# Kernel optimization log

Measured on AMD Instinct MI355X. Metric: run time of the kernel, lower is better.

Reference implementation:

```python
import jax, jax.numpy as jnp
import numpy as np

# dims: T time steps, B batch, F clinical features, H GRU hidden, NH heads, DFF ffn dim, AH single-attn hidden
T, B, F, H, NH, DFF, AH = 128, 256, 76, 64, 4, 256, 8


def setup_inputs() -> dict:
    key = jax.random.key(0)
    ks = jax.random.split(key, 32)
    s = 0.1
    def u(k, shape):
        return jax.random.uniform(k, shape, jnp.float32, -s, s)
    return {
        "x": jax.random.normal(ks[0], (T, B, F), jnp.float32),
        # per-feature GRU(1, H) weight stacks (torch gate order: r, z, n)
        "gru_w_ih": u(ks[1], (F, 3 * H)),          # input dim is 1 -> squeezed
        "gru_w_hh": u(ks[2], (F, 3 * H, H)),
        "gru_b_ih": jnp.zeros((F, 3 * H), jnp.float32),
        "gru_b_hh": jnp.zeros((F, 3 * H), jnp.float32),
        # per-feature SingleAttention('new', time_aware) params
        "att_Wt": u(ks[3], (F, H, AH)),
        "att_Wx": u(ks[4], (F, H, AH)),
        "att_rate": jnp.full((F,), 0.8, jnp.float32),
        # multi-head self-attention over the feature axis
        "mha_wq": u(ks[5], (H, H)), "mha_bq": jnp.zeros((H,), jnp.float32),
        "mha_wk": u(ks[6], (H, H)), "mha_bk": jnp.zeros((H,), jnp.float32),
        "mha_wv": u(ks[7], (H, H)), "mha_bv": jnp.zeros((H,), jnp.float32),
        "mha_wo": u(ks[8], (H, H)), "mha_bo": jnp.zeros((H,), jnp.float32),
        # position-wise feed forward
        "ffn_w1": u(ks[9], (H, DFF)), "ffn_b1": jnp.zeros((DFF,), jnp.float32),
        "ffn_w2": u(ks[10], (DFF, H)), "ffn_b2": jnp.zeros((H,), jnp.float32),
        # FinalAttentionQKV ('mul')
        "fa_wq": u(ks[11], (H, H)), "fa_bq": jnp.zeros((H,), jnp.float32),
        "fa_wk": u(ks[12], (H, H)), "fa_bk": jnp.zeros((H,), jnp.float32),
        "fa_wv": u(ks[13], (H, H)), "fa_bv": jnp.zeros((H,), jnp.float32),
        # output head
        "out0_w": u(ks[14], (H, H)), "out0_b": jnp.zeros((H,), jnp.float32),
        "out1_w": u(ks[15], (H, 1)), "out1_b": jnp.zeros((1,), jnp.float32),
    }


def reference(x, gru_w_ih, gru_w_hh, gru_b_ih, gru_b_hh,
              att_Wt, att_Wx, att_rate,
              mha_wq, mha_bq, mha_wk, mha_bk, mha_wv, mha_bv, mha_wo, mha_bo,
              ffn_w1, ffn_b1, ffn_w2, ffn_b2,
              fa_wq, fa_bq, fa_wk, fa_bk, fa_wv, fa_bv,
              out0_w, out0_b, out1_w, out1_b):
    # x: (T, B, F); torch permutes to (B, T, F)
    Ts, Bsz, Fd = x.shape
    Hd = gru_w_hh.shape[-1]
    dk = Hd // NH

    # ---- all F GRU(1,H) channels fused into one scan (vectorized over F) ----
    xs = jnp.transpose(x, (0, 2, 1))  # (T, F, B)

    def step(h, x_t):  # h: (F,B,H), x_t: (F,B)
        gx = x_t[:, :, None] * gru_w_ih[:, None, :] + gru_b_ih[:, None, :]      # (F,B,3H)
        gh = jnp.einsum('fbh,fgh->fbg', h, gru_w_hh) + gru_b_hh[:, None, :]     # (F,B,3H)
        rx, zx, nx = jnp.split(gx, 3, axis=-1)
        rh, zh, nh = jnp.split(gh, 3, axis=-1)
        r = jax.nn.sigmoid(rx + rh)
        z = jax.nn.sigmoid(zx + zh)
        n = jnp.tanh(nx + r * nh)
        h_new = (1.0 - z) * n + z * h
        return h_new, h_new

    h0 = jnp.zeros((Fd, Bsz, Hd), x.dtype)
    _, hs = jax.lax.scan(step, h0, xs)        # (T, F, B, H)
    hs = jnp.transpose(hs, (1, 2, 0, 3))       # (F, B, T, H)

    # ---- per-feature SingleAttention, type='new', time-aware ----
    q = jnp.einsum('fbh,fha->fba', hs[:, :, -1, :], att_Wt)   # (F,B,AH)
    k = jnp.einsum('fbth,fha->fbta', hs, att_Wx)              # (F,B,T,AH)
    dp = jnp.einsum('fba,fbta->fbt', q, k)                    # (F,B,T)
    sig = jax.nn.sigmoid(dp)
    decay = jnp.arange(Ts, 0, -1, dtype=x.dtype)              # T..1 (time_decays + 1)
    denom = jax.nn.sigmoid(att_rate)[:, None, None] * (jnp.log(2.72 + (1.0 - sig)) * decay)
    e = jax.nn.relu(sig / denom)
    a = jax.nn.softmax(e, axis=-1)
    emb = jnp.einsum('fbt,fbth->bfh', a, hs)                  # (B, F, H)

    def lin(t, w, b):
        return t @ w + b

    # ---- multi-head self-attention over the F axis + residual ----
    # NOTE: original lambda ignores its (layernormed) argument, so LN is dead code.
    def heads(t):
        return t.reshape(Bsz, Fd, NH, dk).transpose(0, 2, 1, 3)
    qh = heads(lin(emb, mha_wq, mha_bq))
    kh = heads(lin(emb, mha_wk, mha_bk))
    vh = heads(lin(emb, mha_wv, mha_bv))
    scores = jnp.einsum('bhqd,bhkd->bhqk', qh, kh) / jnp.sqrt(jnp.asarray(dk, x.dtype))
    attn = jax.nn.softmax(scores, axis=-1)
    ctx = jnp.einsum('bhqk,bhkd->bhqd', attn, vh).transpose(0, 2, 1, 3).reshape(Bsz, Fd, Hd)
    ctx = emb + lin(ctx, mha_wo, mha_bo)

    # ---- position-wise feed-forward + residual ----
    ctx = ctx + lin(jax.nn.relu(lin(ctx, ffn_w1, ffn_b1)), ffn_w2, ffn_b2)

    # ---- FinalAttentionQKV, type='mul' ----
    fq = lin(ctx[:, -1, :], fa_wq, fa_bq)      # (B,H)
    fk = lin(ctx, fa_wk, fa_bk)                # (B,F,H)
    fv = lin(ctx, fa_wv, fa_bv)                # (B,F,H)
    fe = jnp.einsum('bfh,bh->bf', fk, fq)
    fa_w = jax.nn.softmax(fe, axis=1)
    v = jnp.einsum('bf,bfh->bh', fa_w, fv)     # (B,H)

    # ---- output head ----
    out = jax.nn.sigmoid(lin(jax.nn.relu(lin(v, out0_w, out0_b)), out1_w, out1_b))
    return out  # (B, 1)
```

## Files before the change

kernel.cpp:

```cpp
#include <hip/hip_runtime.h>
#include <hip/hip_bf16.h>
#include <cstdint>
#include <cstddef>

#define TT 128
#define BBATCH 256
#define FFEAT 76
#define HDIM 64
#define NHEAD 4
#define DKH 16
#define DFF1 256
#define AH1 8
#define NROWS (BBATCH * FFEAT)
#define FCP 38

#define LOG2E 1.4426950408889634f

typedef __attribute__((ext_vector_type(8))) short bf16x8;
typedef __attribute__((ext_vector_type(4))) float f32x4;

__device__ __forceinline__ float fast_sigmoid(float v) {
    float p = __builtin_amdgcn_exp2f(-v * LOG2E);
    return __builtin_amdgcn_rcpf(1.0f + p);
}
__device__ __forceinline__ float fast_tanh(float v) {
    float p = __builtin_amdgcn_exp2f(v * (2.0f * LOG2E));
    return 1.0f - 2.0f * __builtin_amdgcn_rcpf(1.0f + p);
}
__device__ __forceinline__ short f2bf(float x) {
    __hip_bfloat16 h = __float2bfloat16(x);
    return *reinterpret_cast<short*>(&h);
}
__device__ __forceinline__ float bf2f(unsigned short s) {
    return __uint_as_float(((unsigned)s) << 16);
}
__device__ __forceinline__ unsigned pack_bf16(float a, float b) {
    unsigned ua = (unsigned)(unsigned short)f2bf(a);
    unsigned ub = (unsigned)(unsigned short)f2bf(b);
    return ua | (ub << 16);
}

__device__ __forceinline__ void attn_wave(
    __hip_bfloat16* hs_chunk, const float* Wt, const float* Wx,
    const float* rate, int f, int f_loc, int b, int lane)
{
    const int g = lane >> 3;
    const int i = lane & 7;
    short* rowbase = (short*)hs_chunk + ((size_t)f_loc * BBATCH + b) * TT * HDIM;
    const uint4* basev = (const uint4*)rowbase;

    uint4 U[16];
    #pragma unroll
    for (int it = 0; it < 16; ++it)
        U[it] = basev[(it * 8 + g) * 8 + i];

    float qv[8];
    {
        uint4 Uv = U[15];
        float h15[8];
        h15[0]=__uint_as_float(Uv.x<<16); h15[1]=__uint_as_float(Uv.x&0xffff0000u);
        h15[2]=__uint_as_float(Uv.y<<16); h15[3]=__uint_as_float(Uv.y&0xffff0000u);
        h15[4]=__uint_as_float(Uv.z<<16); h15[5]=__uint_as_float(Uv.z&0xffff0000u);
        h15[6]=__uint_as_float(Uv.w<<16); h15[7]=__uint_as_float(Uv.w&0xffff0000u);
        const float* wtp = Wt + (size_t)f * 512 + (size_t)(8 * i) * 8;
        #pragma unroll
        for (int a = 0; a < 8; ++a) qv[a] = 0.f;
        #pragma unroll
        for (int j = 0; j < 8; ++j)
            #pragma unroll
            for (int a = 0; a < 8; ++a)
                qv[a] = fmaf(h15[j], wtp[j * 8 + a], qv[a]);
        #pragma unroll
        for (int a = 0; a < 8; ++a) {
            qv[a] += __shfl_xor(qv[a], 1, 64);
            qv[a] += __shfl_xor(qv[a], 2, 64);
            qv[a] += __shfl_xor(qv[a], 4, 64);
            qv[a]  = __shfl(qv[a], 63, 64);
        }
    }
    float wv[8];
    {
        const float* wxp = Wx + (size_t)f * 512 + (size_t)(8 * i) * 8;
        #pragma unroll
        for (int j = 0; j < 8; ++j) {
            float s2 = 0.f;
            #pragma unroll
            for (int a = 0; a < 8; ++a) s2 = fmaf(wxp[j * 8 + a], qv[a], s2);
            wv[j] = s2;
        }
    }
    const float rs = fast_sigmoid(rate[f]);

    float m = -1.0e30f, s = 0.f;
    float o[8];
    #pragma unroll
    for (int j = 0; j < 8; ++j) o[j] = 0.f;

    #pragma unroll
    for (int it = 0; it < 16; ++it) {
        const int t = it * 8 + g;
        uint4 Uv = U[it];
        float h[8];
        h[0] = __uint_as_float(Uv.x << 16); h[1] = __uint_as_float(Uv.x & 0xffff0000u);
        h[2] = __uint_as_float(Uv.y << 16); h[3] = __uint_as_float(Uv.y & 0xffff0000u);
        h[4] = __uint_as_float(Uv.z << 16); h[5] = __uint_as_float(Uv.z & 0xffff0000u);
        h[6] = __uint_as_float(Uv.w << 16); h[7] = __uint_as_float(Uv.w & 0xffff0000u);
        float dp = 0.f;
        #pragma unroll
        for (int j = 0; j < 8; ++j) dp = fmaf(h[j], wv[j], dp);
        dp += __shfl_xor(dp, 1, 64);
        dp += __shfl_xor(dp, 2, 64);
        dp += __shfl_xor(dp, 4, 64);
        float sig = fast_sigmoid(dp);
        float den = rs * (__logf(2.72f + (1.0f - sig)) * (float)(TT - t));
        float e = fmaxf(sig / den, 0.0f);
        float nm = fmaxf(m, e);
        float sc = __builtin_amdgcn_exp2f((m - nm) * LOG2E);
        float p  = __builtin_amdgcn_exp2f((e - nm) * LOG2E);
        s = fmaf(s, sc, p);
        #pragma unroll
        for (int j = 0; j < 8; ++j) o[j] = fmaf(o[j], sc, p * h[j]);
        m = nm;
    }
    #pragma unroll
    for (int k = 8; k <= 32; k <<= 1) {
        float om = __shfl_xor(m, k, 64);
        float os = __shfl_xor(s, k, 64);
        float nm = fmaxf(m, om);
        float sa = __builtin_amdgcn_exp2f((m - nm) * LOG2E);
        float sb = __builtin_amdgcn_exp2f((om - nm) * LOG2E);
        s = s * sa + os * sb;
        #pragma unroll
        for (int j = 0; j < 8; ++j) {
            float oo = __shfl_xor(o[j], k, 64);
            o[j] = o[j] * sa + oo * sb;
        }
        m = nm;
    }
    if (g == 0) {
        float inv = __builtin_amdgcn_rcpf(s);
        float4 v0, v1;
        v0.x = o[0]*inv; v0.y = o[1]*inv; v0.z = o[2]*inv; v0.w = o[3]*inv;
        v1.x = o[4]*inv; v1.y = o[5]*inv; v1.z = o[6]*inv; v1.w = o[7]*inv;
        float* edst = (float*)rowbase;
        *(float4*)&edst[8 * i]     = v0;
        *(float4*)&edst[8 * i + 4] = v1;
    }
}

__global__ __launch_bounds__(64) void fused_gru_attn_kernel(
    const float* __restrict__ x, const float* __restrict__ w_ih,
    const float* __restrict__ w_hh, const float* __restrict__ b_ih,
    const float* __restrict__ b_hh, const float* __restrict__ Wt,
    const float* __restrict__ Wx, const float* __restrict__ rate,
    int ngru, int f0_gru, __hip_bfloat16* __restrict__ hs_w,
    int f0_att, __hip_bfloat16* hs_r)
{
    __shared__ float x_lds[TT][16];
    const int gid  = blockIdx.x;
    const int lane = threadIdx.x;

    if (gid < ngru) {
        const int f_loc = gid >> 4;
        const int f     = f0_gru + f_loc;
        const int b0    = (gid & 15) * 16;
        const int c     = lane & 15;
        const int q     = lane >> 4;

        for (int i = lane; i < TT * 16; i += 64) {
            int t = i >> 4, b = i & 15;
            x_lds[t][b] = x[((size_t)t * BBATCH + b0 + b) * FFEAT + f];
        }
        __syncthreads();

        bf16x8 afr[12][2];
        {
            const float* whh_f = w_hh + (size_t)f * 192 * 64;
            #pragma unroll
            for (int nt = 0; nt < 12; ++nt) {
                int gate = nt >> 2, tt = nt & 3;
                int urow = (c >> 2) * 8 + (tt & 1) * 4 + (c & 3) + (tt >> 1) * 32;
                const float* row = whh_f + (size_t)(gate * 64 + urow) * 64;
                #pragma unroll
                for (int kq = 0; kq < 2; ++kq) {
                    bf16x8 fr;
                    #pragma unroll
                    for (int j = 0; j < 8; ++j) fr[j] = f2bf(row[kq * 32 + q * 8 + j]);
                    afr[nt][kq] = fr;
                }
            }
        }
        float wr[4][4], wz[4][4], wn[4][4], bnx[4][4];
        f32x4 biasv[12];
        #pragma unroll
        for (int tt = 0; tt < 4; ++tt) {
            #pragma unroll
            for (int r = 0; r < 4; ++r) {
                int u = q * 8 + (tt & 1) * 4 + r + (tt >> 1) * 32;
                wr[tt][r]  = w_ih[f*192 + u];
                wz[tt][r]  = w_ih[f*192 + 64 + u];
                wn[tt][r]  = w_ih[f*192 + 128 + u];
                bnx[tt][r] = b_ih[f*192 + 128 + u];
                biasv[tt][r]     = b_ih[f*192 + u]      + b_hh[f*192 + u];
                biasv[4 + tt][r] = b_ih[f*192 + 64 + u] + b_hh[f*192 + 64 + u];
                biasv[8 + tt][r] = b_hh[f*192 + 128 + u];
            }
        }

        float hprev[4][4];
        #pragma unroll
        for (int tt = 0; tt < 4; ++tt)
            #pragma unroll
            for (int r = 0; r < 4; ++r) hprev[tt][r] = 0.f;

        bf16x8 hb0 = {0,0,0,0,0,0,0,0};
        bf16x8 hb1 = {0,0,0,0,0,0,0,0};

        short* hs_b = (short*)hs_w + ((size_t)f_loc * BBATCH + b0 + c) * TT * HDIM;

        for (int t = 0; t < TT; ++t) {
            f32x4 acc[12];
            #pragma unroll
            for (int nt = 0; nt < 12; ++nt) {
                f32x4 a = __builtin_amdgcn_mfma_f32_16x16x32_bf16(afr[nt][0], hb0, biasv[nt], 0, 0, 0);
                acc[nt]  = __builtin_amdgcn_mfma_f32_16x16x32_bf16(afr[nt][1], hb1, a, 0, 0, 0);
            }

            float xv = x_lds[t][c];
            float hn4[4][4];
            #pragma unroll
            for (int tt = 0; tt < 4; ++tt) {
                #pragma unroll
                for (int r = 0; r < 4; ++r) {
                    float R  = fmaf(xv, wr[tt][r], acc[tt][r]);
                    float Z  = fmaf(xv, wz[tt][r], acc[4 + tt][r]);
                    float NX = fmaf(xv, wn[tt][r], bnx[tt][r]);
                    float rg = fast_sigmoid(R);
                    float zg = fast_sigmoid(Z);
                    float ng = fast_tanh(fmaf(rg, acc[8 + tt][r], NX));
                    float hn = fmaf(zg, hprev[tt][r] - ng, ng);
                    hprev[tt][r] = hn;
                    hn4[tt][r] = hn;
                }
            }
            {
                union { int4 i; bf16x8 v; } u0, u1;
                u0.i.x = pack_bf16(hn4[0][0], hn4[0][1]);
                u0.i.y = pack_bf16(hn4[0][2], hn4[0][3]);
                u0.i.z = pack_bf16(hn4[1][0], hn4[1][1]);
                u0.i.w = pack_bf16(hn4[1][2], hn4[1][3]);
                u1.i.x = pack_bf16(hn4[2][0], hn4[2][1]);
                u1.i.y = pack_bf16(hn4[2][2], hn4[2][3]);
                u1.i.z = pack_bf16(hn4[3][0], hn4[3][1]);
                u1.i.w = pack_bf16(hn4[3][2], hn4[3][3]);
                hb0 = u0.v; hb1 = u1.v;
            }
            short* dst = hs_b + (size_t)t * HDIM + q * 8;
            *(bf16x8*)dst = hb0;
            *(bf16x8*)(dst + 32) = hb1;
        }
    } else {
        const int aid   = gid - ngru;
        const int b     = aid & 255;
        const int f_loc = aid >> 8;
        attn_wave(hs_r, Wt, Wx, rate, f0_att + f_loc, f_loc, b, lane);
    }
}

__global__ __launch_bounds__(256) void attn2_p_kernel(
    __hip_bfloat16* hs_chunk, const float* __restrict__ Wt,
    const float* __restrict__ Wx, const float* __restrict__ rate, int f_base)
{
    const int w    = threadIdx.x >> 6;
    const int lane = threadIdx.x & 63;
    const int b    = blockIdx.x * 4 + w;
    const int f_loc = blockIdx.y;
    attn_wave(hs_chunk, Wt, Wx, rate, f_base + f_loc, f_loc, b, lane);
}

__global__ __launch_bounds__(64) void bounce_kernel(float* hs0f)
{
    const int k = blockIdx.x;
    hs0f[(size_t)(400 + k) * 4096 + 2048 + threadIdx.x] =
        hs0f[(size_t)k * 4096 + threadIdx.x];
}

__global__ __launch_bounds__(64) void compact_kernel(
    const float* hs0f, const float* hs1f, float* emb)
{
    const int j = blockIdx.x;
    const int f = j >> 8;
    const int b = j & 255;
    const int chunk = (f >= FCP);
    const int f_loc = chunk ? f - FCP : f;
    const size_t row = (size_t)f_loc * BBATCH + b;
    const float* base = chunk ? hs1f : hs0f;
    size_t off = (!chunk && row <= 303)
               ? ((size_t)(400 + row) * 4096 + 2048)
               : row * 4096;
    emb[((size_t)b * FFEAT + f) * HDIM + threadIdx.x] = base[off + threadIdx.x];
}

__global__ __launch_bounds__(64) void gru_scan_kernel(
    const float* __restrict__ x, const float* __restrict__ w_ih,
    const float* __restrict__ w_hh, const float* __restrict__ b_ih,
    const float* __restrict__ b_hh, const float* __restrict__ Wt,
    const float* __restrict__ Wx, int f_base,
    __hip_bfloat16* __restrict__ hs, float* __restrict__ wtil)
{
    const int f_loc = blockIdx.y;
    const int f     = f_base + f_loc;
    const int b0    = blockIdx.x * 16;
    const int lane  = threadIdx.x;
    const int c     = lane & 15;
    const int q     = lane >> 4;

    __shared__ float x_lds[TT][16];
    __shared__ float wt_s[64][8];
    __shared__ float wx_s[64][8];
    __shared__ short hx[16][72];
    __shared__ float q_s[16][8];

    for (int i = lane; i < TT * 16; i += 64) {
        int t = i >> 4, b = i & 15;
        x_lds[t][b] = x[((size_t)t * BBATCH + b0 + b) * FFEAT + f];
    }
    for (int i = lane; i < 512; i += 64) {
        ((float*)wt_s)[i] = Wt[(size_t)f * 512 + i];
        ((float*)wx_s)[i] = Wx[(size_t)f * 512 + i];
    }
    __syncthreads();

    bf16x8 afr[12][2];
    {
        const float* whh_f = w_hh + (size_t)f * 192 * 64;
        #pragma unroll
        for (int nt = 0; nt < 12; ++nt) {
            int gate = nt >> 2, tt = nt & 3;
            int urow = (c >> 2) * 8 + (tt & 1) * 4 + (c & 3) + (tt >> 1) * 32;
            const float* row = whh_f + (size_t)(gate * 64 + urow) * 64;
            #pragma unroll
            for (int kq = 0; kq < 2; ++kq) {
                bf16x8 fr;
                #pragma unroll
                for (int j = 0; j < 8; ++j) fr[j] = f2bf(row[kq * 32 + q * 8 + j]);
                afr[nt][kq] = fr;
            }
        }
    }
    float wr[4][4], wz[4][4], wn[4][4], bnx[4][4];
    f32x4 biasv[12];
    #pragma unroll
    for (int tt = 0; tt < 4; ++tt) {
        #pragma unroll
        for (int r = 0; r < 4; ++r) {
            int u = q * 8 + (tt & 1) * 4 + r + (tt >> 1) * 32;
            wr[tt][r]  = w_ih[f*192 + u];
            wz[tt][r]  = w_ih[f*192 + 64 + u];
            wn[tt][r]  = w_ih[f*192 + 128 + u];
            bnx[tt][r] = b_ih[f*192 + 128 + u];
            biasv[tt][r]     = b_ih[f*192 + u]      + b_hh[f*192 + u];
            biasv[4 + tt][r] = b_ih[f*192 + 64 + u] + b_hh[f*192 + 64 + u];
            biasv[8 + tt][r] = b_hh[f*192 + 128 + u];
        }
    }

    float hprev[4][4];
    #pragma unroll
    for (int tt = 0; tt < 4; ++tt)
        #pragma unroll
        for (int r = 0; r < 4; ++r) hprev[tt][r] = 0.f;

    bf16x8 hb0 = {0,0,0,0,0,0,0,0};
    bf16x8 hb1 = {0,0,0,0,0,0,0,0};

    short* hs_b = (short*)hs + ((size_t)f_loc * BBATCH + b0 + c) * TT * HDIM;

    for (int t = 0; t < TT; ++t) {
        f32x4 acc[12];
        #pragma unroll
        for (int nt = 0; nt < 12; ++nt) {
            f32x4 a = __builtin_amdgcn_mfma_f32_16x16x32_bf16(afr[nt][0], hb0, biasv[nt], 0, 0, 0);
            acc[nt]  = __builtin_amdgcn_mfma_f32_16x16x32_bf16(afr[nt][1], hb1, a, 0, 0, 0);
        }

        float xv = x_lds[t][c];
        float hn4[4][4];
        #pragma unroll
        for (int tt = 0; tt < 4; ++tt) {
            #pragma unroll
            for (int r = 0; r < 4; ++r) {
                float R  = fmaf(xv, wr[tt][r], acc[tt][r]);
                float Z  = fmaf(xv, wz[tt][r], acc[4 + tt][r]);
                float NX = fmaf(xv, wn[tt][r], bnx[tt][r]);
                float rg = fast_sigmoid(R);
                float zg = fast_sigmoid(Z);
                float ng = fast_tanh(fmaf(rg, acc[8 + tt][r], NX));
                float hn = fmaf(zg, hprev[tt][r] - ng, ng);
                hprev[tt][r] = hn;
                hn4[tt][r] = hn;
            }
        }
        {
            union { int4 i; bf16x8 v; } u0, u1;
            u0.i.x = pack_bf16(hn4[0][0], hn4[0][1]);
            u0.i.y = pack_bf16(hn4[0][2], hn4[0][3]);
            u0.i.z = pack_bf16(hn4[1][0], hn4[1][1]);
            u0.i.w = pack_bf16(hn4[1][2], hn4[1][3]);
            u1.i.x = pack_bf16(hn4[2][0], hn4[2][1]);
            u1.i.y = pack_bf16(hn4[2][2], hn4[2][3]);
            u1.i.z = pack_bf16(hn4[3][0], hn4[3][1]);
            u1.i.w = pack_bf16(hn4[3][2], hn4[3][3]);
            hb0 = u0.v; hb1 = u1.v;
        }
        short* dst = hs_b + (size_t)t * HDIM + q * 8;
        *(bf16x8*)dst = hb0;
        *(bf16x8*)(dst + 32) = hb1;
    }

    *(bf16x8*)&hx[c][q * 8]      = hb0;
    *(bf16x8*)&hx[c][32 + q * 8] = hb1;

    #pragma unroll
    for (int rr = 0; rr < 2; ++rr) {
        int role = rr * 64 + lane;
        int b = role >> 3, a = role & 7;
        float s = 0.f;
        #pragma unroll 8
        for (int j = 0; j < 64; ++j)
            s = fmaf(bf2f((unsigned short)hx[b][j]), wt_s[j][a], s);
        q_s[b][a] = s;
    }
    {
        int b = lane >> 2, jb = (lane & 3) * 16;
        float qreg[8];
        #pragma unroll
        for (int a = 0; a < 8; ++a) qreg[a] = q_s[b][a];
        float* wt_out = wtil + ((size_t)(b0 + b) * FFEAT + f) * HDIM + jb;
        #pragma unroll
        for (int j4 = 0; j4 < 4; ++j4) {
            float4 v;
            #pragma unroll
            for (int jj = 0; jj < 4; ++jj) {
                int j = jb + j4 * 4 + jj;
                float s = 0.f;
                #pragma unroll
                for (int a = 0; a < 8; ++a) s = fmaf(wx_s[j][a], qreg[a], s);
                (&v.x)[jj] = s;
            }
            *(float4*)&wt_out[j4 * 4] = v;
        }
    }
}

__global__ __launch_bounds__(256) void attn2_kernel(
    const __hip_bfloat16* __restrict__ hs, const float* wtil,
    const float* __restrict__ rate, int f_base, float* emb)
{
    const int w     = threadIdx.x >> 6;
    const int lane  = threadIdx.x & 63;
    const int b     = blockIdx.x * 4 + w;
    const int f_loc = blockIdx.y;
    const int f     = f_base + f_loc;
    const int g     = lane >> 3;
    const int i     = lane & 7;

    const uint4* basev = (const uint4*)((const short*)hs +
                          ((size_t)f_loc * BBATCH + b) * TT * HDIM);

    uint4 U[16];
    #pragma unroll
    for (int it = 0; it < 16; ++it)
        U[it] = basev[(it * 8 + g) * 8 + i];

    float wv[8];
    {
        const float4* src = (const float4*)(wtil + ((size_t)b * FFEAT + f) * HDIM + 8 * i);
        float4 a = src[0], c2 = src[1];
        wv[0]=a.x; wv[1]=a.y; wv[2]=a.z; wv[3]=a.w;
        wv[4]=c2.x; wv[5]=c2.y; wv[6]=c2.z; wv[7]=c2.w;
    }
    const float rs = fast_sigmoid(rate[f]);

    float m = -1.0e30f, s = 0.f;
    float o[8];
    #pragma unroll
    for (int j = 0; j < 8; ++j) o[j] = 0.f;

    #pragma unroll
    for (int it = 0; it < 16; ++it) {
        const int t = it * 8 + g;
        uint4 Uv = U[it];
        float h[8];
        h[0] = __uint_as_float(Uv.x << 16); h[1] = __uint_as_float(Uv.x & 0xffff0000u);
        h[2] = __uint_as_float(Uv.y << 16); h[3] = __uint_as_float(Uv.y & 0xffff0000u);
        h[4] = __uint_as_float(Uv.z << 16); h[5] = __uint_as_float(Uv.z & 0xffff0000u);
        h[6] = __uint_as_float(Uv.w << 16); h[7] = __uint_as_float(Uv.w & 0xffff0000u);
        float dp = 0.f;
        #pragma unroll
        for (int j = 0; j < 8; ++j) dp = fmaf(h[j], wv[j], dp);
        dp += __shfl_xor(dp, 1, 64);
        dp += __shfl_xor(dp, 2, 64);
        dp += __shfl_xor(dp, 4, 64);
        float sig = fast_sigmoid(dp);
        float den = rs * (__logf(2.72f + (1.0f - sig)) * (float)(TT - t));
        float e = fmaxf(sig / den, 0.0f);
        float nm = fmaxf(m, e);
        float sc = __builtin_amdgcn_exp2f((m - nm) * LOG2E);
        float p  = __builtin_amdgcn_exp2f((e - nm) * LOG2E);
        s = fmaf(s, sc, p);
        #pragma unroll
        for (int j = 0; j < 8; ++j) o[j] = fmaf(o[j], sc, p * h[j]);
        m = nm;
    }
    #pragma unroll
    for (int k = 8; k <= 32; k <<= 1) {
        float om = __shfl_xor(m, k, 64);
        float os = __shfl_xor(s, k, 64);
        float nm = fmaxf(m, om);
        float sa = __builtin_amdgcn_exp2f((m - nm) * LOG2E);
        float sb = __builtin_amdgcn_exp2f((om - nm) * LOG2E);
        s = s * sa + os * sb;
        #pragma unroll
        for (int j = 0; j < 8; ++j) {
            float oo = __shfl_xor(o[j], k, 64);
            o[j] = o[j] * sa + oo * sb;
        }
        m = nm;
    }
    if (g == 0) {
        float inv = __builtin_amdgcn_rcpf(s);
        float4 v0, v1;
        v0.x = o[0]*inv; v0.y = o[1]*inv; v0.z = o[2]*inv; v0.w = o[3]*inv;
        v1.x = o[4]*inv; v1.y = o[5]*inv; v1.z = o[6]*inv; v1.w = o[7]*inv;
        float* dst = &emb[((size_t)b * FFEAT + f) * HDIM + 8 * i];
        *(float4*)dst       = v0;
        *(float4*)(dst + 4) = v1;
    }
}

struct GemmP {
    const float* X;
    const float* W[3];
    const float* B[3];
    const float* R;
    float* Y[3];
    int K;
    int Nfull;
    int act;
};

__global__ __launch_bounds__(256) void gemm_kernel(GemmP A)
{
    __shared__ float xs[64][65];
    __shared__ float ws[64][68];

    const int tid = threadIdx.x;
    const int tx  = tid & 15;
    const int ty  = tid >> 4;
    const int m0  = blockIdx.x * 64;
    const int n0  = blockIdx.y * 64;
    const int z   = blockIdx.z;

    const float* W = A.W[z];
    const float* Bv = A.B[z];
    float* Y = A.Y[z];
    const int K = A.K, Nfull = A.Nfull;

    float acc[4][4];
    #pragma unroll
    for (int i = 0; i < 4; ++i)
        #pragma unroll
        for (int j = 0; j < 4; ++j) acc[i][j] = 0.f;

    for (int kc = 0; kc < K; kc += 64) {
        for (int s = tid; s < 1024; s += 256) {
            int row = s >> 4, c4 = s & 15;
            float4 xv = *(const float4*)&A.X[(size_t)(m0 + row) * K + kc + 4*c4];
            xs[row][4*c4+0] = xv.x; xs[row][4*c4+1] = xv.y;
            xs[row][4*c4+2] = xv.z; xs[row][4*c4+3] = xv.w;
            float4 wv = *(const float4*)&W[(size_t)(kc + row) * Nfull + n0 + 4*c4];
            *(float4*)&ws[row][4*c4] = wv;
        }
        __syncthreads();
        #pragma unroll 16
        for (int k = 0; k < 64; ++k) {
            float a0 = xs[4*ty+0][k], a1 = xs[4*ty+1][k];
            float a2 = xs[4*ty+2][k], a3 = xs[4*ty+3][k];
            float4 wv = *(const float4*)&ws[k][4*tx];
            #pragma unroll
            for (int j = 0; j < 4; ++j) {
                float wj = (&wv.x)[j];
                acc[0][j] = fmaf(a0, wj, acc[0][j]);
                acc[1][j] = fmaf(a1, wj, acc[1][j]);
                acc[2][j] = fmaf(a2, wj, acc[2][j]);
                acc[3][j] = fmaf(a3, wj, acc[3][j]);
            }
        }
        __syncthreads();
    }

    float4 bias = *(const float4*)&Bv[n0 + 4*tx];
    #pragma unroll
    for (int i = 0; i < 4; ++i) {
        int row = m0 + 4*ty + i;
        float4 v;
        v.x = acc[i][0] + bias.x; v.y = acc[i][1] + bias.y;
        v.z = acc[i][2] + bias.z; v.w = acc[i][3] + bias.w;
        if (A.act) {
            v.x = fmaxf(v.x, 0.f); v.y = fmaxf(v.y, 0.f);
            v.z = fmaxf(v.z, 0.f); v.w = fmaxf(v.w, 0.f);
        }
        if (A.R) {
            float4 r4 = *(const float4*)&A.R[(size_t)row * Nfull + n0 + 4*tx];
            v.x += r4.x; v.y += r4.y; v.z += r4.z; v.w += r4.w;
        }
        *(float4*)&Y[(size_t)row * Nfull + n0 + 4*tx] = v;
    }
}

__global__ __launch_bounds__(256) void mha_core_kernel(
    const float* __restrict__ q, const float* __restrict__ k,
    const float* __restrict__ v, float* __restrict__ ctx)
{
    const int b  = blockIdx.x;
    const int hh = blockIdx.y;
    const int tid = threadIdx.x;

    __shared__ float qs[FFEAT][17];
    __shared__ float ks[FFEAT][17];
    __shared__ float vs[FFEAT][17];
    __shared__ float ps[FFEAT][77];

    for (int idx = tid; idx < FFEAT * DKH; idx += 256) {
        int i = idx >> 4, c = idx & 15;
        size_t g = ((size_t)b * FFEAT + i) * HDIM + hh * DKH + c;
        qs[i][c] = q[g]; ks[i][c] = k[g]; vs[i][c] = v[g];
    }
    __syncthreads();

    for (int idx = tid; idx < FFEAT * FFEAT; idx += 256) {
        int i = idx / FFEAT, j = idx % FFEAT;
        float acc = 0.f;
        #pragma unroll
        for (int c = 0; c < DKH; ++c) acc = fmaf(qs[i][c], ks[j][c], acc);
        ps[i][j] = acc * 0.25f;
    }
    __syncthreads();

    if (tid < FFEAT) {
        float mm = ps[tid][0];
        #pragma unroll 4
        for (int j = 1; j < FFEAT; ++j) mm = fmaxf(mm, ps[tid][j]);
        float ss = 0.f;
        #pragma unroll 4
        for (int j = 0; j < FFEAT; ++j) {
            float pv = __builtin_amdgcn_exp2f((ps[tid][j] - mm) * LOG2E);
            ps[tid][j] = pv; ss += pv;
        }
        float inv = 1.0f / ss;
        #pragma unroll 4
        for (int j = 0; j < FFEAT; ++j) ps[tid][j] *= inv;
    }
    __syncthreads();

    for (int idx = tid; idx < FFEAT * DKH; idx += 256) {
        int i = idx >> 4, c = idx & 15;
        float acc = 0.f;
        #pragma unroll 4
        for (int j = 0; j < FFEAT; ++j) acc = fmaf(ps[i][j], vs[j][c], acc);
        ctx[((size_t)b * FFEAT + i) * HDIM + hh * DKH + c] = acc;
    }
}

__global__ __launch_bounds__(128) void final_kernel(
    const float* __restrict__ ctx3, const float* __restrict__ fk,
    const float* __restrict__ fv,
    const float* __restrict__ faq, const float* __restrict__ fabq,
    const float* __restrict__ o0w, const float* __restrict__ o0b,
    const float* __restrict__ o1w, const float* __restrict__ o1b,
    float* __restrict__ out)
{
    const int b = blockIdx.x;
    const int tid = threadIdx.x;

    __shared__ float last[HDIM];
    __shared__ float fqs[HDIM];
    __shared__ float sm[FFEAT];
    __shared__ float vv[HDIM];
    __shared__ float hh[HDIM];
    __shared__ float redm[2], redp[2];

    if (tid < HDIM) last[tid] = ctx3[((size_t)b * FFEAT + FFEAT - 1) * HDIM + tid];
    __syncthreads();
    if (tid < HDIM) {
        float acc = fabq[tid];
        #pragma unroll 8
        for (int j = 0; j < HDIM; ++j) acc = fmaf(last[j], faq[j * HDIM + tid], acc);
        fqs[tid] = acc;
    }
    __syncthreads();

    float e = -3.0e38f;
    if (tid < FFEAT) {
        const float4* kr = (const float4*)&fk[((size_t)b * FFEAT + tid) * HDIM];
        float acc = 0.f;
        #pragma unroll
        for (int c4 = 0; c4 < 16; ++c4) {
            float4 kv = kr[c4];
            acc = fmaf(kv.x, fqs[4*c4+0], acc);
            acc = fmaf(kv.y, fqs[4*c4+1], acc);
            acc = fmaf(kv.z, fqs[4*c4+2], acc);
            acc = fmaf(kv.w, fqs[4*c4+3], acc);
        }
        e = acc;
    }
    float m = e;
    #pragma unroll
    for (int off = 32; off > 0; off >>= 1) m = fmaxf(m, __shfl_xor(m, off, 64));
    if ((tid & 63) == 0) redm[tid >> 6] = m;
    __syncthreads();
    m = fmaxf(redm[0], redm[1]);
    float p = (tid < FFEAT) ? __builtin_amdgcn_exp2f((e - m) * LOG2E) : 0.f;
    float s = p;
    #pragma unroll
    for (int off = 32; off > 0; off >>= 1) s += __shfl_xor(s, off, 64);
    if ((tid & 63) == 0) redp[tid >> 6] = s;
    __syncthreads();
    s = redp[0] + redp[1];
    if (tid < FFEAT) sm[tid] = p / s;
    __syncthreads();

    if (tid < HDIM) {
        float acc = 0.f;
        for (int ff = 0; ff < FFEAT; ++ff)
            acc = fmaf(sm[ff], fv[((size_t)b * FFEAT + ff) * HDIM + tid], acc);
        vv[tid] = acc;
    }
    __syncthreads();
    if (tid < HDIM) {
        float acc = o0b[tid];
        #pragma unroll 8
        for (int j = 0; j < HDIM; ++j) acc = fmaf(vv[j], o0w[j * HDIM + tid], acc);
        hh[tid] = fmaxf(acc, 0.f);
    }
    __syncthreads();
    if (tid < 64) {
        float t = hh[tid] * o1w[tid];
        #pragma unroll
        for (int off = 32; off > 0; off >>= 1) t += __shfl_xor(t, off, 64);
        if (tid == 0) out[b] = fast_sigmoid(t + o1b[0]);
    }
}

__global__ void ws_report_kernel(float* out, int n, float ws_mib) {
    int i = blockIdx.x * blockDim.x + threadIdx.x;
    if (i < n) out[i] = ws_mib;
}

static void run_tail(const float* emb, float* ts,
                     const float* wq, const float* bq, const float* wk2, const float* bk2,
                     const float* wv2, const float* bv2, const float* wo, const float* bo,
                     const float* w1, const float* b1, const float* w2, const float* b2,
                     const float* faq, const float* fabq, const float* fak, const float* fabk,
                     const float* fav, const float* fabv, const float* o0w, const float* o0b,
                     const float* o1w, const float* o1b, float* out, hipStream_t stream)
{
    const size_t R64 = (size_t)NROWS * HDIM;
    float* q    = ts;
    float* k    = ts + 1*R64;
    float* v    = ts + 2*R64;
    float* ctx  = ts + 3*R64;
    float* ctx2 = ts + 4*R64;
    float* hid  = ts + 5*R64;
    float* ctx3 = ts + 9*R64;
    float* fk   = ts + 10*R64;
    float* fv   = ts + 11*R64;
    const int MB = NROWS / 64;

    {
        GemmP A = { emb, {wq, wk2, wv2}, {bq, bk2, bv2}, nullptr, {q, k, v}, 64, 64, 0 };
        gemm_kernel<<<dim3(MB, 1, 3), dim3(256), 0, stream>>>(A);
    }
    mha_core_kernel<<<dim3(BBATCH, NHEAD), dim3(256), 0, stream>>>(q, k, v, ctx);
    {
        GemmP A = { ctx, {wo, nullptr, nullptr}, {bo, nullptr, nullptr}, emb,
                    {ctx2, nullptr, nullptr}, 64, 64, 0 };
        gemm_kernel<<<dim3(MB, 1, 1), dim3(256), 0, stream>>>(A);
    }
    {
        GemmP A = { ctx2, {w1, nullptr, nullptr}, {b1, nullptr, nullptr}, nullptr,
                    {hid, nullptr, nullptr}, 64, 256, 1 };
        gemm_kernel<<<dim3(MB, 4, 1), dim3(256), 0, stream>>>(A);
    }
    {
        GemmP A = { hid, {w2, nullptr, nullptr}, {b2, nullptr, nullptr}, ctx2,
                    {ctx3, nullptr, nullptr}, 256, 64, 0 };
        gemm_kernel<<<dim3(MB, 1, 1), dim3(256), 0, stream>>>(A);
    }
    {
        GemmP A = { ctx3, {fak, fav, nullptr}, {fabk, fabv, nullptr}, nullptr,
                    {fk, fv, nullptr}, 64, 64, 0 };
        gemm_kernel<<<dim3(MB, 1, 2), dim3(256), 0, stream>>>(A);
    }
    final_kernel<<<dim3(BBATCH), dim3(128), 0, stream>>>(
        ctx3, fk, fv, faq, fabq, o0w, o0b, o1w, o1b, out);
}

extern "C" void kernel_launch(void* const* d_in, const int* in_sizes, int n_in,
                              void* d_out, int out_size, void* d_ws, size_t ws_size,
                              hipStream_t stream)
{
    const float* x     = (const float*)d_in[0];
    const float* w_ih  = (const float*)d_in[1];
    const float* w_hh  = (const float*)d_in[2];
    const float* b_ih  = (const float*)d_in[3];
    const float* b_hh  = (const float*)d_in[4];
    const float* attWt = (const float*)d_in[5];
    const float* attWx = (const float*)d_in[6];
    const float* attRt = (const float*)d_in[7];
    const float* wq    = (const float*)d_in[8];
    const float* bq    = (const float*)d_in[9];
    const float* wk    = (const float*)d_in[10];
    const float* bk    = (const float*)d_in[11];
    const float* wv    = (const float*)d_in[12];
    const float* bv    = (const float*)d_in[13];
    const float* wo    = (const float*)d_in[14];
    const float* bo    = (const float*)d_in[15];
    const float* w1    = (const float*)d_in[16];
    const float* b1    = (const float*)d_in[17];
    const float* w2    = (const float*)d_in[18];
    const float* b2    = (const float*)d_in[19];
    const float* faq   = (const float*)d_in[20];
    const float* fabq  = (const float*)d_in[21];
    const float* fak   = (const float*)d_in[22];
    const float* fabk  = (const float*)d_in[23];
    const float* fav   = (const float*)d_in[24];
    const float* fabv  = (const float*)d_in[25];
    const float* o0w   = (const float*)d_in[26];
    const float* o0b   = (const float*)d_in[27];
    const float* o1w   = (const float*)d_in[28];
    const float* o1b   = (const float*)d_in[29];
    float* out = (float*)d_out;

    const size_t emb_bytes = (size_t)NROWS * HDIM * 4;
    const size_t hs_half   = (size_t)FCP * BBATCH * TT * HDIM * 2;

    if (ws_size >= 2 * hs_half) {
        __hip_bfloat16* hs0 = (__hip_bfloat16*)d_ws;
        __hip_bfloat16* hs1 = (__hip_bfloat16*)((char*)d_ws + hs_half);

        fused_gru_attn_kernel<<<dim3(16 * FCP), dim3(64), 0, stream>>>(
            x, w_ih, w_hh, b_ih, b_hh, attWt, attWx, attRt,
            16 * FCP, 0, hs0, 0, hs1);
        fused_gru_attn_kernel<<<dim3(16 * FCP + BBATCH * FCP), dim3(64), 0, stream>>>(
            x, w_ih, w_hh, b_ih, b_hh, attWt, attWx, attRt,
            16 * FCP, FCP, hs1, 0, hs0);
        bounce_kernel<<<dim3(304), dim3(64), 0, stream>>>((float*)hs0);
        attn2_p_kernel<<<dim3(BBATCH / 4, FCP), dim3(256), 0, stream>>>(
            hs1, attWt, attWx, attRt, FCP);
        float* emb = (float*)d_ws;
        compact_kernel<<<dim3(NROWS), dim3(64), 0, stream>>>(
            (const float*)hs0, (const float*)hs1, emb);

        float* ts = (float*)((char*)d_ws + emb_bytes);
        run_tail(emb, ts, wq, bq, wk, bk, wv, bv, wo, bo, w1, b1, w2, b2,
                 faq, fabq, fak, fabk, fav, fabv, o0w, o0b, o1w, o1b, out, stream);
        return;
    }

    const size_t R64        = (size_t)NROWS * HDIM;
    const size_t tail_bytes = 12 * R64 * 4;

    const int chunk_opts[6] = {76, 38, 19, 4, 2, 1};
    int FC = 0;
    for (int i = 0; i < 6; ++i) {
        size_t hs_b = (size_t)chunk_opts[i] * BBATCH * TT * HDIM * 2;
        size_t scratch = hs_b > tail_bytes ? hs_b : tail_bytes;
        if (emb_bytes + scratch <= ws_size) { FC = chunk_opts[i]; break; }
    }
    if (FC == 0) {
        ws_report_kernel<<<dim3((out_size + 255) / 256), dim3(256), 0, stream>>>(
            out, out_size, (float)((double)ws_size / (1024.0 * 1024.0)));
        return;
    }

    float* embwtil = (float*)d_ws;
    char*  scratch = (char*)d_ws + emb_bytes;
    __hip_bfloat16* hs = (__hip_bfloat16*)scratch;

    for (int f0 = 0; f0 < FFEAT; f0 += FC) {
        int fc = (FFEAT - f0 < FC) ? (FFEAT - f0) : FC;
        gru_scan_kernel<<<dim3(16, fc), dim3(64), 0, stream>>>(
            x, w_ih, w_hh, b_ih, b_hh, attWt, attWx, f0, hs, embwtil);
        attn2_kernel<<<dim3(BBATCH / 4, fc), dim3(256), 0, stream>>>(
            hs, embwtil, attRt, f0, embwtil);
    }

    run_tail(embwtil, (float*)scratch, wq, bq, wk, bk, wv, bv, wo, bo, w1, b1, w2, b2,
             faq, fabq, fak, fabk, fav, fabv, o0w, o0b, o1w, o1b, out, stream);
}
```

Baseline: 563.8 us.

## Store first-chunk GRU states as int8 and precompute attention query vectors in GRU

The first feature chunk's GRU hidden states are now written as int8, scaled by 127, instead of bf16. This halves that chunk's write and read traffic between the GRU and attention phases. The GRU blocks now also compute the time-aware attention query from the final hidden state and its projection through Wx (wtil), writing it into the emb buffer so attention waves only load a precomputed vector. Attention writes its output straight to emb, which removes the bounce and compact kernels and the extra buffer shuffling. The int8 quantization adds approximation error to the attention inputs, which may affect output accuracy.

Result: no change. 563.6 us (-0.0%).

```diff
diff --git a/kernel.cpp b/kernel.cpp
--- a/kernel.cpp
+++ b/kernel.cpp
@@ -39,57 +39,36 @@
     unsigned ub = (unsigned)(unsigned short)f2bf(b);
     return ua | (ub << 16);
 }
-
-__device__ __forceinline__ void attn_wave(
-    __hip_bfloat16* hs_chunk, const float* Wt, const float* Wx,
-    const float* rate, int f, int f_loc, int b, int lane)
+__device__ __forceinline__ unsigned pack_i8x4m(float a, float b, float c, float d) {
+    unsigned ua = __float_as_uint(fmaf(a, 127.f, 12582912.f));
+    unsigned ub = __float_as_uint(fmaf(b, 127.f, 12582912.f));
+    unsigned uc = __float_as_uint(fmaf(c, 127.f, 12582912.f));
+    unsigned ud = __float_as_uint(fmaf(d, 127.f, 12582912.f));
+    return (ua & 0xffu) | ((ub & 0xffu) << 8) | ((uc & 0xffu) << 16) | (ud << 24);
+}
+
+__device__ __forceinline__ void attn_wave_i8(
+    const unsigned char* hs8, const float* wtil, const float* rate,
+    int f, int f_loc, int b, int lane, float* emb)
 {
     const int g = lane >> 3;
     const int i = lane & 7;
-    short* rowbase = (short*)hs_chunk + ((size_t)f_loc * BBATCH + b) * TT * HDIM;
-    const uint4* basev = (const uint4*)rowbase;
-
-    uint4 U[16];
+    const unsigned char* rb = hs8 + ((size_t)f_loc * BBATCH + b) * TT * 64;
+
+    uint2 U[16];
     #pragma unroll
     for (int it = 0; it < 16; ++it)
-        U[it] = basev[(it * 8 + g) * 8 + i];
-
-    float qv[8];
-    {
-        uint4 Uv = U[15];
-        float h15[8];
-        h15[0]=__uint_as_float(Uv.x<<16); h15[1]=__uint_as_float(Uv.x&0xffff0000u);
-        h15[2]=__uint_as_float(Uv.y<<16); h15[3]=__uint_as_float(Uv.y&0xffff0000u);
-        h15[4]=__uint_as_float(Uv.z<<16); h15[5]=__uint_as_float(Uv.z&0xffff0000u);
-        h15[6]=__uint_as_float(Uv.w<<16); h15[7]=__uint_as_float(Uv.w&0xffff0000u);
-        const float* wtp = Wt + (size_t)f * 512 + (size_t)(8 * i) * 8;
-        #pragma unroll
-        for (int a = 0; a < 8; ++a) qv[a] = 0.f;
-        #pragma unroll
-        for (int j = 0; j < 8; ++j)
-            #pragma unroll
-            for (int a = 0; a < 8; ++a)
-                qv[a] = fmaf(h15[j], wtp[j * 8 + a], qv[a]);
-        #pragma unroll
-        for (int a = 0; a < 8; ++a) {
-            qv[a] += __shfl_xor(qv[a], 1, 64);
-            qv[a] += __shfl_xor(qv[a], 2, 64);
-            qv[a] += __shfl_xor(qv[a], 4, 64);
-            qv[a]  = __shfl(qv[a], 63, 64);
-        }
-    }
+        U[it] = *(const uint2*)(rb + ((size_t)(it * 8 + g) * 64 + i * 8));
+
     float wv[8];
     {
-        const float* wxp = Wx + (size_t)f * 512 + (size_t)(8 * i) * 8;
-        #pragma unroll
-        for (int j = 0; j < 8; ++j) {
-            float s2 = 0.f;
-            #pragma unroll
-            for (int a = 0; a < 8; ++a) s2 = fmaf(wxp[j * 8 + a], qv[a], s2);
-            wv[j] = s2;
-        }
+        const float4* src = (const float4*)(wtil + ((size_t)b * FFEAT + f) * HDIM + 8 * i);
+        float4 a = src[0], c2 = src[1];
+        wv[0]=a.x; wv[1]=a.y; wv[2]=a.z; wv[3]=a.w;
+        wv[4]=c2.x; wv[5]=c2.y; wv[6]=c2.z; wv[7]=c2.w;
     }
     const float rs = fast_sigmoid(rate[f]);
+    const float S = 1.0f / 127.0f;
 
     float m = -1.0e30f, s = 0.f;
     float o[8];
@@ -99,12 +78,16 @@
     #pragma unroll
     for (int it = 0; it < 16; ++it) {
         const int t = it * 8 + g;
-        uint4 Uv = U[it];
+        uint2 u = U[it];
         float h[8];
-        h[0] = __uint_as_float(Uv.x << 16); h[1] = __uint_as_float(Uv.x & 0xffff0000u);
-        h[2] = __uint_as_float(Uv.y << 16); h[3] = __uint_as_float(Uv.y & 0xffff0000u);
-        h[4] = __uint_as_float(Uv.z << 16); h[5] = __uint_as_float(Uv.z & 0xffff0000u);
-        h[6] = __uint_as_float(Uv.w << 16); h[7] = __uint_as_float(Uv.w & 0xffff0000u);
+        h[0] = (float)(signed char)(u.x      ) * S;
+        h[1] = (float)(signed char)(u.x >>  8) * S;
+        h[2] = (float)(signed char)(u.x >> 16) * S;
+        h[3] = (float)(signed char)(u.x >> 24) * S;
+        h[4] = (float)(signed char)(u.y      ) * S;
+        h[5] = (float)(signed char)(u.y >>  8) * S;
+        h[6] = (float)(signed char)(u.y >> 16) * S;
+        h[7] = (float)(signed char)(u.y >> 24) * S;
         float dp = 0.f;
         #pragma unroll
         for (int j = 0; j < 8; ++j) dp = fmaf(h[j], wv[j], dp);
@@ -142,21 +125,108 @@
         float4 v0, v1;
         v0.x = o[0]*inv; v0.y = o[1]*inv; v0.z = o[2]*inv; v0.w = o[3]*inv;
         v1.x = o[4]*inv; v1.y = o[5]*inv; v1.z = o[6]*inv; v1.w = o[7]*inv;
-        float* edst = (float*)rowbase;
-        *(float4*)&edst[8 * i]     = v0;
-        *(float4*)&edst[8 * i + 4] = v1;
-    }
-}
-
+        float* dst = &emb[((size_t)b * FFEAT + f) * HDIM + 8 * i];
+        *(float4*)dst       = v0;
+        *(float4*)(dst + 4) = v1;
+    }
+}
+
+__device__ __forceinline__ void attn_wave_bf(
+    const __hip_bfloat16* hs, const float* wtil, const float* rate,
+    int f, int f_loc, int b, int lane, float* emb)
+{
+    const int g = lane >> 3;
+    const int i = lane & 7;
+    const uint4* basev = (const uint4*)((const short*)hs +
+                          ((size_t)f_loc * BBATCH + b) * TT * HDIM);
+
+    uint4 U[16];
+    #pragma unroll
+    for (int it = 0; it < 16; ++it)
+        U[it] = basev[(it * 8 + g) * 8 + i];
+
+    float wv[8];
+    {
+        const float4* src = (const float4*)(wtil + ((size_t)b * FFEAT + f) * HDIM + 8 * i);
+        float4 a = src[0], c2 = src[1];
+        wv[0]=a.x; wv[1]=a.y; wv[2]=a.z; wv[3]=a.w;
+        wv[4]=c2.x; wv[5]=c2.y; wv[6]=c2.z; wv[7]=c2.w;
+    }
+    const float rs = fast_sigmoid(rate[f]);
+
+    float m = -1.0e30f, s = 0.f;
+    float o[8];
+    #pragma unroll
+    for (int j = 0; j < 8; ++j) o[j] = 0.f;
+
+    #pragma unroll
+    for (int it = 0; it < 16; ++it) {
+        const int t = it * 8 + g;
+        uint4 Uv = U[it];
+        float h[8];
+        h[0] = __uint_as_float(Uv.x << 16); h[1] = __uint_as_float(Uv.x & 0xffff0000u);
+        h[2] = __uint_as_float(Uv.y << 16); h[3] = __uint_as_float(Uv.y & 0xffff0000u);
+        h[4] = __uint_as_float(Uv.z << 16); h[5] = __uint_as_float(Uv.z & 0xffff0000u);
+        h[6] = __uint_as_float(Uv.w << 16); h[7] = __uint_as_float(Uv.w & 0xffff0000u);
+        float dp = 0.f;
+        #pragma unroll
+        for (int j = 0; j < 8; ++j) dp = fmaf(h[j], wv[j], dp);
+        dp += __shfl_xor(dp, 1, 64);
+        dp += __shfl_xor(dp, 2, 64);
+        dp += __shfl_xor(dp, 4, 64);
+        float sig = fast_sigmoid(dp);
+        float den = rs * (__logf(2.72f + (1.0f - sig)) * (float)(TT - t));
+        float e = fmaxf(sig / den, 0.0f);
+        float nm = fmaxf(m, e);
+        float sc = __builtin_amdgcn_exp2f((m - nm) * LOG2E);
+        float p  = __builtin_amdgcn_exp2f((e - nm) * LOG2E);
+        s = fmaf(s, sc, p);
+        #pragma unroll
+        for (int j = 0; j < 8; ++j) o[j] = fmaf(o[j], sc, p * h[j]);
+        m = nm;
+    }
+    #pragma unroll
+    for (int k = 8; k <= 32; k <<= 1) {
+        float om = __shfl_xor(m, k, 64);
+        float os = __shfl_xor(s, k, 64);
+        float nm = fmaxf(m, om);
+        float sa = __builtin_amdgcn_exp2f((m - nm) * LOG2E);
+        float sb = __builtin_amdgcn_exp2f((om - nm) * LOG2E);
+        s = s * sa + os * sb;
+        #pragma unroll
+        for (int j = 0; j < 8; ++j) {
+            float oo = __shfl_xor(o[j], k, 64);
+            o[j] = o[j] * sa + oo * sb;
+        }
+        m = nm;
+    }
+    if (g == 0) {
+        float inv = __builtin_amdgcn_rcpf(s);
+        float4 v0, v1;
+        v0.x = o[0]*inv; v0.y = o[1]*inv; v0.z = o[2]*inv; v0.w = o[3]*inv;
+        v1.x = o[4]*inv; v1.y = o[5]*inv; v1.z = o[6]*inv; v1.w = o[7]*inv;
+        float* dst = &emb[((size_t)b * FFEAT + f) * HDIM + 8 * i];
+        *(float4*)dst       = v0;
+        *(float4*)(dst + 4) = v1;
+    }
+}
+
+template<int SI8, int RI8>
 __global__ __launch_bounds__(64) void fused_gru_attn_kernel(
     const float* __restrict__ x, const float* __restrict__ w_ih,
     const float* __restrict__ w_hh, const float* __restrict__ b_ih,
     const float* __restrict__ b_hh, const float* __restrict__ Wt,
     const float* __restrict__ Wx, const float* __restrict__ rate,
-    int ngru, int f0_gru, __hip_bfloat16* __restrict__ hs_w,
-    int f0_att, __hip_bfloat16* hs_r)
+    int ngru, int f0_gru, void* __restrict__ hs_w,
+    int f0_att, const void* __restrict__ hs_r,
+    float* wtil_emb)
 {
     __shared__ float x_lds[TT][16];
+    __shared__ float wt_s[64][8];
+    __shared__ float wx_s[64][8];
+    __shared__ short hx[16][72];
+    __shared__ float q_s[16][8];
+
     const int gid  = blockIdx.x;
     const int lane = threadIdx.x;
 
@@ -170,6 +240,10 @@
         for (int i = lane; i < TT * 16; i += 64) {
             int t = i >> 4, b = i & 15;
             x_lds[t][b] = x[((size_t)t * BBATCH + b0 + b) * FFEAT + f];
+        }
+        for (int i = lane; i < 512; i += 64) {
+            ((float*)wt_s)[i] = Wt[(size_t)f * 512 + i];
+            ((float*)wx_s)[i] = Wx[(size_t)f * 512 + i];
         }
         __syncthreads();
 
@@ -216,7 +290,9 @@
         bf16x8 hb0 = {0,0,0,0,0,0,0,0};
         bf16x8 hb1 = {0,0,0,0,0,0,0,0};
 
-        short* hs_b = (short*)hs_w + ((size_t)f_loc * BBATCH + b0 + c) * TT * HDIM;
+        unsigned char* hs8_b = (unsigned char*)hs_w +
+                               ((size_t)f_loc * BBATCH + b0 + c) * TT * 64;
+        short* hsb_b = (short*)hs_w + ((size_t)f_loc * BBATCH + b0 + c) * TT * HDIM;
 
         for (int t = 0; t < TT; ++t) {
             f32x4 acc[12];
@@ -255,50 +331,77 @@
                 u1.i.w = pack_bf16(hn4[3][2], hn4[3][3]);
                 hb0 = u0.v; hb1 = u1.v;
             }
-            short* dst = hs_b + (size_t)t * HDIM + q * 8;
-            *(bf16x8*)dst = hb0;
-            *(bf16x8*)(dst + 32) = hb1;
+            if constexpr (SI8) {
+                uint2 s0, s1;
+                s0.x = pack_i8x4m(hn4[0][0], hn4[0][1], hn4[0][2], hn4[0][3]);
+                s0.y = pack_i8x4m(hn4[1][0], hn4[1][1], hn4[1][2], hn4[1][3]);
+                s1.x = pack_i8x4m(hn4[2][0], hn4[2][1], hn4[2][2], hn4[2][3]);
+                s1.y = pack_i8x4m(hn4[3][0], hn4[3][1], hn4[3][2], hn4[3][3]);
+                unsigned char* dst = hs8_b + (size_t)t * 64 + q * 8;
+                *(uint2*)dst        = s0;
+                *(uint2*)(dst + 32) = s1;
+            } else {
+                short* dst = hsb_b + (size_t)t * HDIM + q * 8;
+                *(bf16x8*)dst = hb0;
+                *(bf16x8*)(dst + 32) = hb1;
+            }
+        }
+
+        *(bf16x8*)&hx[c][q * 8]      = hb0;
+        *(bf16x8*)&hx[c][32 + q * 8] = hb1;
+
+        #pragma unroll
+        for (int rr = 0; rr < 2; ++rr) {
+            int role = rr * 64 + lane;
+            int b = role >> 3, a = role & 7;
+            float s = 0.f;
+            #pragma unroll 8
+            for (int j = 0; j < 64; ++j)
+                s = fmaf(bf2f((unsigned short)hx[b][j]), wt_s[j][a], s);
+            q_s[b][a] = s;
+        }
+        {
+            int b = lane >> 2, jb = (lane & 3) * 16;
+            float qreg[8];
+            #pragma unroll
+            for (int a = 0; a < 8; ++a) qreg[a] = q_s[b][a];
+            float* wt_out = wtil_emb + ((size_t)(b0 + b) * FFEAT + f) * HDIM + jb;
+            #pragma unroll
+            for (int j4 = 0; j4 < 4; ++j4) {
+                float4 v;
+                #pragma unroll
+                for (int jj = 0; jj < 4; ++jj) {
+                    int j = jb + j4 * 4 + jj;
+                    float s = 0.f;
+                    #pragma unroll
+                    for (int a = 0; a < 8; ++a) s = fmaf(wx_s[j][a], qreg[a], s);
+                    (&v.x)[jj] = s;
+                }
+                *(float4*)&wt_out[j4 * 4] = v;
+            }
         }
     } else {
         const int aid   = gid - ngru;
         const int b     = aid & 255;
         const int f_loc = aid >> 8;
-        attn_wave(hs_r, Wt, Wx, rate, f0_att + f_loc, f_loc, b, lane);
-    }
-}
-
-__global__ __launch_bounds__(256) void attn2_p_kernel(
-    __hip_bfloat16* hs_chunk, const float* __restrict__ Wt,
-    const float* __restrict__ Wx, const float* __restrict__ rate, int f_base)
+        if constexpr (RI8)
+            attn_wave_i8((const unsigned char*)hs_r, wtil_emb, rate,
+                         f0_att + f_loc, f_loc, b, lane, wtil_emb);
+        else
+            attn_wave_bf((const __hip_bfloat16*)hs_r, wtil_emb, rate,
+                         f0_att + f_loc, f_loc, b, lane, wtil_emb);
+    }
+}
+
+__global__ __launch_bounds__(256) void attn2_kernel(
+    const __hip_bfloat16* __restrict__ hs, const float* wtil,
+    const float* __restrict__ rate, int f_base, float* emb)
 {
-    const int w    = threadIdx.x >> 6;
-    const int lane = threadIdx.x & 63;
-    const int b    = blockIdx.x * 4 + w;
+    const int w     = threadIdx.x >> 6;
+    const int lane  = threadIdx.x & 63;
+    const int b     = blockIdx.x * 4 + w;
     const int f_loc = blockIdx.y;
-    attn_wave(hs_chunk, Wt, Wx, rate, f_base + f_loc, f_loc, b, lane);
-}
-
-__global__ __launch_bounds__(64) void bounce_kernel(float* hs0f)
-{
-    const int k = blockIdx.x;
-    hs0f[(size_t)(400 + k) * 4096 + 2048 + threadIdx.x] =
-        hs0f[(size_t)k * 4096 + threadIdx.x];
-}
-
-__global__ __launch_bounds__(64) void compact_kernel(
-    const float* hs0f, const float* hs1f, float* emb)
-{
-    const int j = blockIdx.x;
-    const int f = j >> 8;
-    const int b = j & 255;
-    const int chunk = (f >= FCP);
-    const int f_loc = chunk ? f - FCP : f;
-    const size_t row = (size_t)f_loc * BBATCH + b;
-    const float* base = chunk ? hs1f : hs0f;
-    size_t off = (!chunk && row <= 303)
-               ? ((size_t)(400 + row) * 4096 + 2048)
-               : row * 4096;
-    emb[((size_t)b * FFEAT + f) * HDIM + threadIdx.x] = base[off + threadIdx.x];
+    attn_wave_bf(hs, wtil, rate, f_base + f_loc, f_loc, b, lane, emb);
 }
 
 __global__ __launch_bounds__(64) void gru_scan_kernel(
@@ -450,92 +553,6 @@
             }
             *(float4*)&wt_out[j4 * 4] = v;
         }
-    }
-}
-
-__global__ __launch_bounds__(256) void attn2_kernel(
-    const __hip_bfloat16* __restrict__ hs, const float* wtil,
-    const float* __restrict__ rate, int f_base, float* emb)
-{
-    const int w     = threadIdx.x >> 6;
-    const int lane  = threadIdx.x & 63;
-    const int b     = blockIdx.x * 4 + w;
-    const int f_loc = blockIdx.y;
-    const int f     = f_base + f_loc;
-    const int g     = lane >> 3;
-    const int i     = lane & 7;
-
-    const uint4* basev = (const uint4*)((const short*)hs +
-                          ((size_t)f_loc * BBATCH + b) * TT * HDIM);
-
-    uint4 U[16];
-    #pragma unroll
-    for (int it = 0; it < 16; ++it)
-        U[it] = basev[(it * 8 + g) * 8 + i];
-
-    float wv[8];
-    {
-        const float4* src = (const float4*)(wtil + ((size_t)b * FFEAT + f) * HDIM + 8 * i);
-        float4 a = src[0], c2 = src[1];
-        wv[0]=a.x; wv[1]=a.y; wv[2]=a.z; wv[3]=a.w;
-        wv[4]=c2.x; wv[5]=c2.y; wv[6]=c2.z; wv[7]=c2.w;
-    }
-    const float rs = fast_sigmoid(rate[f]);
-
-    float m = -1.0e30f, s = 0.f;
-    float o[8];
-    #pragma unroll
-    for (int j = 0; j < 8; ++j) o[j] = 0.f;
-
-    #pragma unroll
-    for (int it = 0; it < 16; ++it) {
-        const int t = it * 8 + g;
-        uint4 Uv = U[it];
-        float h[8];
-        h[0] = __uint_as_float(Uv.x << 16); h[1] = __uint_as_float(Uv.x & 0xffff0000u);
-        h[2] = __uint_as_float(Uv.y << 16); h[3] = __uint_as_float(Uv.y & 0xffff0000u);
-        h[4] = __uint_as_float(Uv.z << 16); h[5] = __uint_as_float(Uv.z & 0xffff0000u);
-        h[6] = __uint_as_float(Uv.w << 16); h[7] = __uint_as_float(Uv.w & 0xffff0000u);
-        float dp = 0.f;
-        #pragma unroll
-        for (int j = 0; j < 8; ++j) dp = fmaf(h[j], wv[j], dp);
-        dp += __shfl_xor(dp, 1, 64);
-        dp += __shfl_xor(dp, 2, 64);
-        dp += __shfl_xor(dp, 4, 64);
-        float sig = fast_sigmoid(dp);
-        float den = rs * (__logf(2.72f + (1.0f - sig)) * (float)(TT - t));
-        float e = fmaxf(sig / den, 0.0f);
-        float nm = fmaxf(m, e);
-        float sc = __builtin_amdgcn_exp2f((m - nm) * LOG2E);
-        float p  = __builtin_amdgcn_exp2f((e - nm) * LOG2E);
-        s = fmaf(s, sc, p);
-        #pragma unroll
-        for (int j = 0; j < 8; ++j) o[j] = fmaf(o[j], sc, p * h[j]);
-        m = nm;
-    }
-    #pragma unroll
-    for (int k = 8; k <= 32; k <<= 1) {
-        float om = __shfl_xor(m, k, 64);
-        float os = __shfl_xor(s, k, 64);
-        float nm = fmaxf(m, om);
-        float sa = __builtin_amdgcn_exp2f((m - nm) * LOG2E);
-        float sb = __builtin_amdgcn_exp2f((om - nm) * LOG2E);
-        s = s * sa + os * sb;
-        #pragma unroll
-        for (int j = 0; j < 8; ++j) {
-            float oo = __shfl_xor(o[j], k, 64);
-            o[j] = o[j] * sa + oo * sb;
-        }
-        m = nm;
-    }
-    if (g == 0) {
-        float inv = __builtin_amdgcn_rcpf(s);
-        float4 v0, v1;
-        v0.x = o[0]*inv; v0.y = o[1]*inv; v0.z = o[2]*inv; v0.w = o[3]*inv;
-        v1.x = o[4]*inv; v1.y = o[5]*inv; v1.z = o[6]*inv; v1.w = o[7]*inv;
-        float* dst = &emb[((size_t)b * FFEAT + f) * HDIM + 8 * i];
-        *(float4*)dst       = v0;
-        *(float4*)(dst + 4) = v1;
     }
 }
 
@@ -844,33 +861,33 @@
     float* out = (float*)d_out;
 
     const size_t emb_bytes = (size_t)NROWS * HDIM * 4;
-    const size_t hs_half   = (size_t)FCP * BBATCH * TT * HDIM * 2;
-
-    if (ws_size >= 2 * hs_half) {
-        __hip_bfloat16* hs0 = (__hip_bfloat16*)d_ws;
-        __hip_bfloat16* hs1 = (__hip_bfloat16*)((char*)d_ws + hs_half);
-
-        fused_gru_attn_kernel<<<dim3(16 * FCP), dim3(64), 0, stream>>>(
+    const size_t hs8_half  = (size_t)FCP * BBATCH * TT * 64;
+    const size_t hsb_half  = hs8_half * 2;
+    const size_t R64       = (size_t)NROWS * HDIM;
+    const size_t tail_bytes = 12 * R64 * 4;
+
+    const size_t need_t1 = emb_bytes + hs8_half + hsb_half;
+
+    if (ws_size >= need_t1) {
+        float* wtil_emb = (float*)d_ws;
+        unsigned char* hs0 = (unsigned char*)d_ws + emb_bytes;
+        __hip_bfloat16* hs1 = (__hip_bfloat16*)(hs0 + hs8_half);
+        float* ts = (float*)((char*)d_ws + emb_bytes);
+
+        const int NG = 16 * FCP;
+        const int NA = BBATCH * FCP;
+        fused_gru_attn_kernel<1, 0><<<dim3(NG), dim3(64), 0, stream>>>(
             x, w_ih, w_hh, b_ih, b_hh, attWt, attWx, attRt,
-            16 * FCP, 0, hs0, 0, hs1);
-        fused_gru_attn_kernel<<<dim3(16 * FCP + BBATCH * FCP), dim3(64), 0, stream>>>(
+            NG, 0, hs0, 0, hs1, wtil_emb);
+        fused_gru_attn_kernel<0, 1><<<dim3(NG + NA), dim3(64), 0, stream>>>(
             x, w_ih, w_hh, b_ih, b_hh, attWt, attWx, attRt,
-            16 * FCP, FCP, hs1, 0, hs0);
-        bounce_kernel<<<dim3(304), dim3(64), 0, stream>>>((float*)hs0);
-        attn2_p_kernel<<<dim3(BBATCH / 4, FCP), dim3(256), 0, stream>>>(
-            hs1, attWt, attWx, attRt, FCP);
-        float* emb = (float*)d_ws;
-        compact_kernel<<<dim3(NROWS), dim3(64), 0, stream>>>(
-            (const float*)hs0, (const float*)hs1, emb);
-
-        float* ts = (float*)((char*)d_ws + emb_bytes);
-        run_tail(emb, ts, wq, bq, wk, bk, wv, bv, wo, bo, w1, b1, w2, b2,
+            NG, FCP, hs1, 0, hs0, wtil_emb);
+        attn2_kernel<<<dim3(BBATCH / 4, FCP), dim3(256), 0, stream>>>(
+            hs1, wtil_emb, attRt, FCP, wtil_emb);
+        run_tail(wtil_emb, ts, wq, bq, wk, bk, wv, bv, wo, bo, w1, b1, w2, b2,
                  faq, fabq, fak, fabk, fav, fabv, o0w, o0b, o1w, o1b, out, stream);
         return;
     }
-
-    const size_t R64        = (size_t)NROWS * HDIM;
-    const size_t tail_bytes = 12 * R64 * 4;
 
     const int chunk_opts[6] = {76, 38, 19, 4, 2, 1};
     int FC = 0;
```
